# Optimization experiments

Measured on AMD Instinct MI355X. Metric: run time of the kernel, lower is better.

Reference implementation:

```python
import jax, jax.numpy as jnp
import numpy as np

N_SPANS = 2000
D_SPAN = 1220          # span representation dim (Test_Encoder docstring)
P = 65536              # number of (mention, antecedent) pairs
D_PHI = 60             # dist(20) + genre(20) + speaker(20)
IN_SIZE = 3 * D_SPAN + D_PHI  # 3720
HID = 150
BINS = np.array([1, 2, 3, 4, 5, 8, 16, 32, 64])


def setup_inputs() -> dict:
    key = jax.random.key(0)
    ks = jax.random.split(key, 16)
    inp = {
        "g_i": jax.random.normal(ks[0], (N_SPANS, D_SPAN), dtype=jnp.float32),
        "s_m": jax.random.normal(ks[1], (N_SPANS,), dtype=jnp.float32),
        "mention_ids": jax.random.randint(ks[2], (P,), 0, N_SPANS, dtype=jnp.int32),
        "antecedent_ids": jax.random.randint(ks[3], (P,), 0, N_SPANS, dtype=jnp.int32),
        "distances": jax.random.randint(ks[4], (P,), 1, 512, dtype=jnp.int32),
        "genres": jax.random.randint(ks[5], (P,), 0, 7, dtype=jnp.int32),
        "speakers": jax.random.randint(ks[6], (P,), 0, 3, dtype=jnp.int32),
        # embedding tables
        "dist_emb": jax.random.normal(ks[7], (len(BINS), 20), dtype=jnp.float32) * 0.1,
        "genre_emb": jax.random.normal(ks[8], (7, 20), dtype=jnp.float32) * 0.1,
        "speaker_emb": jax.random.normal(ks[9], (3, 20), dtype=jnp.float32) * 0.1,
        # FFNN params (fc1, fc2, fc3)
        "W1": jax.random.normal(ks[10], (IN_SIZE, HID), dtype=jnp.float32) / np.sqrt(IN_SIZE),
        "b1": jnp.zeros((HID,), dtype=jnp.float32),
        "W2": jax.random.normal(ks[11], (HID, HID), dtype=jnp.float32) / np.sqrt(HID),
        "b2": jnp.zeros((HID,), dtype=jnp.float32),
        "W3": jax.random.normal(ks[12], (HID, 1), dtype=jnp.float32) / np.sqrt(HID),
        "b3": jnp.zeros((1,), dtype=jnp.float32),
    }
    return inp


def _dist_to_bin(distances):
    # replicate Span_Distance_Embedding.dist_to_bin_id: bin id s.t. bins[id] <= d < bins[id+1],
    # last bin catches everything else (including d < 1, per the Python fallthrough).
    bins = jnp.asarray(BINS, dtype=jnp.int32)
    ids = jnp.searchsorted(bins, distances, side="right") - 1
    return jnp.clip(ids, 0, len(BINS) - 1)


def reference(g_i, s_m, mention_ids, antecedent_ids, distances, genres, speakers,
              dist_emb, genre_emb, speaker_emb, W1, b1, W2, b2, W3, b3):
    # phi_ij: concat of distance / genre / speaker embeddings   [P, 60]
    phi = jnp.concatenate(
        [dist_emb[_dist_to_bin(distances)], genre_emb[genres], speaker_emb[speakers]],
        axis=1)
    vec_i = g_i[mention_ids]        # [P, D]
    vec_j = g_i[antecedent_ids]     # [P, D]
    x = jnp.concatenate([vec_i, vec_j, vec_j * vec_j, phi], axis=1)  # [P, 3D+60]
    # FFNN (dropout inactive at eval)
    h = jax.nn.relu(x @ W1 + b1)
    h = jax.nn.relu(h @ W2 + b2)
    s_ij = (h @ W3 + b3)[:, 0]      # [P]
    coref_scores = s_m[mention_ids] + s_m[antecedent_ids] + s_ij
    return coref_scores
```

## Files before the change

### kernel.cpp

```cpp
#include <hip/hip_runtime.h>

typedef short bf16x8 __attribute__((ext_vector_type(8)));
typedef short bf16x4 __attribute__((ext_vector_type(4)));
typedef float f32x4  __attribute__((ext_vector_type(4)));

#define NSPAN 2000
#define DSPAN 1220
#define NPAIR 65536
#define HID   150
#define HP    160
#define TW    320
#define NKS   78
#define NKH   39
#define NMT   128
#define NNT   20
#define KC    6
#define NCMB  189

#define GA 1248
#define GB 390
#define GC 119
#define GD 13
#define GE 160

static __device__ __forceinline__ short f2bf(float x) {
  unsigned u = __builtin_bit_cast(unsigned, x);
  u = (u + 0x7FFFu + ((u >> 16) & 1u)) >> 16;
  return (short)u;
}

__global__ __launch_bounds__(256)
void prep_all(const float* __restrict__ g, const float* __restrict__ W1,
              const float* __restrict__ b1, const float* __restrict__ de,
              const float* __restrict__ ge, const float* __restrict__ se,
              const float* __restrict__ W2, short* __restrict__ A_fr,
              short* __restrict__ Wc_fr, float* __restrict__ combo,
              short* __restrict__ W2_fr, float* __restrict__ T) {
  int b = blockIdx.x;
  int t = threadIdx.x;
  if (b < GA) {
    int tid = b * 256 + t;
    int l  = tid & 63;
    int t2 = tid >> 6;
    int ks = t2 % NKH;
    int mt = t2 / NKH;
    int m  = mt * 16 + (l & 15);
    int k0 = ks * 32 + ((l >> 4) << 3);
    float x[8];
    if (m < NSPAN && k0 + 8 <= DSPAN) {
      float4 f0 = *(const float4*)&g[m * DSPAN + k0];
      float4 f1 = *(const float4*)&g[m * DSPAN + k0 + 4];
      x[0]=f0.x; x[1]=f0.y; x[2]=f0.z; x[3]=f0.w;
      x[4]=f1.x; x[5]=f1.y; x[6]=f1.z; x[7]=f1.w;
    } else {
#pragma unroll
      for (int i = 0; i < 8; ++i) {
        int k = k0 + i;
        x[i] = (m < NSPAN && k < DSPAN) ? g[m * DSPAN + k] : 0.f;
      }
    }
    short v1[8], v2[8];
#pragma unroll
    for (int i = 0; i < 8; ++i) { v1[i] = f2bf(x[i]); v2[i] = f2bf(x[i] * x[i]); }
    size_t o1 = ((size_t)(mt * NKS + ks) * 64 + l) * 8;
    *(bf16x8*)(A_fr + o1) = *(const bf16x8*)v1;
    *(bf16x8*)(A_fr + o1 + (size_t)NKH * 512) = *(const bf16x8*)v2;
  } else if (b < GA + GB) {
    int tid = (b - GA) * 256 + t;
    int l  = tid & 63;
    int t2 = tid >> 6;
    int ks = t2 % NKS;
    int nt = t2 / NKS;
    int n  = nt * 16 + (l & 15);
    int k0 = ks * 32 + ((l >> 4) << 3);
    short v[8];
#pragma unroll
    for (int i = 0; i < 8; ++i) {
      int k = k0 + i;
      float x = 0.f;
      if (n < HID) {
        if (k < DSPAN)                     x = W1[k * HID + n];
      } else if (n >= HP && n < HP + HID) {
        int j = n - HP;
        if (k < DSPAN)                     x = W1[(DSPAN + k) * HID + j];
        else if (k >= 1248 && k < 2468)    x = W1[(1192 + k) * HID + j];
      }
      v[i] = f2bf(x);
    }
    *(bf16x8*)(Wc_fr + (size_t)tid * 8) = *(const bf16x8*)v;
  } else if (b < GA + GB + GC) {
    int idx = (b - GA - GB) * 256 + t;
    if (idx < NCMB * HP) {
      int c = idx / HP;
      int j = idx - c * HP;
      float v = 0.f;
      if (j < HID) {
        int si = c % 3;
        int t2 = c / 3;
        int gi = t2 % 7;
        int bi = t2 / 7;
        v = b1[j];
        const float* dp = de + bi * 20;
        const float* gp = ge + gi * 20;
        const float* sp = se + si * 20;
#pragma unroll
        for (int e = 0; e < 20; ++e) {
          v += dp[e] * W1[(3660 + e) * HID + j];
          v += gp[e] * W1[(3680 + e) * HID + j];
          v += sp[e] * W1[(3700 + e) * HID + j];
        }
      }
      combo[idx] = v;
    }
  } else if (b < GA + GB + GC + GD) {
    int tid = (b - GA - GB - GC) * 256 + t;
    if (tid < 3200) {
      int l  = tid & 63;
      int t2 = tid >> 6;
      int ks = t2 % 5;
      int jt = t2 / 5;
      int n  = jt * 16 + (l & 15);
      int k0 = ks * 32 + ((l >> 4) << 3);
      short v[8];
#pragma unroll
      for (int i = 0; i < 8; ++i) {
        int k = k0 + i;
        float x = (k < HID && n < HID) ? W2[k * HID + n] : 0.f;
        v[i] = f2bf(x);
      }
      *(bf16x8*)(W2_fr + (size_t)tid * 8) = *(const bf16x8*)v;
    }
  } else {
    int idx = (b - GA - GB - GC - GD) * 256 + t;
    f32x4 z = {0.f, 0.f, 0.f, 0.f};
    if (idx < NSPAN * TW / 4) ((f32x4*)T)[idx] = z;
  }
}

__global__ __launch_bounds__(256)
void span_gemm(const short* __restrict__ A_fr, const short* __restrict__ Wc_fr,
               float* __restrict__ T) {
  int t = threadIdx.x, w = t >> 6, l = t & 63;
  int mt  = blockIdx.y * 4 + w;
  int ntb = blockIdx.x * 4;
  int ksb = blockIdx.z * 13;
  const short* pa = A_fr + ((size_t)(mt * NKS + ksb) * 64 + l) * 8;
  const short* pb = Wc_fr + ((size_t)(ntb * NKS + ksb) * 64 + l) * 8;
  f32x4 a0 = {0.f, 0.f, 0.f, 0.f}, a1 = a0, a2 = a0, a3 = a0;
#pragma unroll
  for (int ks = 0; ks < 13; ++ks) {
    bf16x8 a  = *(const bf16x8*)pa;
    bf16x8 b0 = *(const bf16x8*)pb;
    bf16x8 b1 = *(const bf16x8*)(pb + (size_t)NKS * 512);
    bf16x8 b2 = *(const bf16x8*)(pb + (size_t)2 * NKS * 512);
    bf16x8 b3 = *(const bf16x8*)(pb + (size_t)3 * NKS * 512);
    a0 = __builtin_amdgcn_mfma_f32_16x16x32_bf16(a, b0, a0, 0, 0, 0);
    a1 = __builtin_amdgcn_mfma_f32_16x16x32_bf16(a, b1, a1, 0, 0, 0);
    a2 = __builtin_amdgcn_mfma_f32_16x16x32_bf16(a, b2, a2, 0, 0, 0);
    a3 = __builtin_amdgcn_mfma_f32_16x16x32_bf16(a, b3, a3, 0, 0, 0);
    pa += 512; pb += 512;
  }
  int col = l & 15, row4 = (l >> 4) << 2;
  f32x4 acc[4] = {a0, a1, a2, a3};
#pragma unroll
  for (int r = 0; r < 4; ++r) {
    int m = mt * 16 + row4 + r;
    if (m < NSPAN) {
#pragma unroll
      for (int j = 0; j < 4; ++j)
        atomicAdd(&T[m * TW + (ntb + j) * 16 + col], acc[j][r]);
    }
  }
}

__global__ __launch_bounds__(256)
void pair_kernel(const float* __restrict__ T, const float* __restrict__ combo,
                 const short* __restrict__ W2_fr,
                 const float* __restrict__ b2, const float* __restrict__ W3,
                 const float* __restrict__ b3, const float* __restrict__ s_m,
                 const int* __restrict__ m_ids, const int* __restrict__ a_ids,
                 const int* __restrict__ dist, const int* __restrict__ genre,
                 const int* __restrict__ spk, float* __restrict__ out) {
  __shared__ float w3s[HP], b2s[HP], sm2[64];

  int t = threadIdx.x, w = t >> 6, l = t & 63;
  int base = blockIdx.x * 64;

  if (t < 64) {
    int p = base + t;
    sm2[t] = s_m[m_ids[p]] + s_m[a_ids[p]];
  }
  if (t < HP) {
    w3s[t] = (t < HID) ? W3[t] : 0.f;
    b2s[t] = (t < HID) ? b2[t] : 0.f;
  }
  float b3v = b3[0];
  __syncthreads();

  int pr = l & 15;
  int q  = l >> 4;
  int p  = base + w * 16 + pr;
  int m = m_ids[p], a = a_ids[p];
  int d = dist[p];
  int bb = (d >= 2) + (d >= 3) + (d >= 4) + (d >= 5) + (d >= 8) +
           (d >= 16) + (d >= 32) + (d >= 64);
  int co = ((bb * 7 + genre[p]) * 3 + spk[p]) * HP;

  const float* pA = T + m * TW + q * 8;
  const float* pB = T + a * TW + HP + q * 8;
  const float* pC = combo + co + q * 8;

  bf16x8 af[5];
#pragma unroll
  for (int ks = 0; ks < 5; ++ks) {
    float4 va0 = *(const float4*)(pA + ks * 32);
    float4 va1 = *(const float4*)(pA + ks * 32 + 4);
    float4 vb0 = *(const float4*)(pB + ks * 32);
    float4 vb1 = *(const float4*)(pB + ks * 32 + 4);
    float4 vc0 = *(const float4*)(pC + ks * 32);
    float4 vc1 = *(const float4*)(pC + ks * 32 + 4);
    short v[8];
    v[0] = f2bf(fmaxf(va0.x + vb0.x + vc0.x, 0.f));
    v[1] = f2bf(fmaxf(va0.y + vb0.y + vc0.y, 0.f));
    v[2] = f2bf(fmaxf(va0.z + vb0.z + vc0.z, 0.f));
    v[3] = f2bf(fmaxf(va0.w + vb0.w + vc0.w, 0.f));
    v[4] = f2bf(fmaxf(va1.x + vb1.x + vc1.x, 0.f));
    v[5] = f2bf(fmaxf(va1.y + vb1.y + vc1.y, 0.f));
    v[6] = f2bf(fmaxf(va1.z + vb1.z + vc1.z, 0.f));
    v[7] = f2bf(fmaxf(va1.w + vb1.w + vc1.w, 0.f));
    af[ks] = *(const bf16x8*)v;
  }

  f32x4 acc[10];
#pragma unroll
  for (int jt = 0; jt < 10; ++jt) acc[jt] = {0.f, 0.f, 0.f, 0.f};

  const short* pw = W2_fr + l * 8;
#pragma unroll
  for (int jt = 0; jt < 10; ++jt) {
#pragma unroll
    for (int ks = 0; ks < 5; ++ks) {
      bf16x8 bfr = *(const bf16x8*)(pw + (size_t)(jt * 5 + ks) * 512);
      acc[jt] = __builtin_amdgcn_mfma_f32_16x16x32_bf16(af[ks], bfr, acc[jt], 0, 0, 0);
    }
  }

  float part[4] = {0.f, 0.f, 0.f, 0.f};
  int cl = l & 15;
#pragma unroll
  for (int jt = 0; jt < 10; ++jt) {
    int n = jt * 16 + cl;
    float w3v = w3s[n], b2v = b2s[n];
#pragma unroll
    for (int r = 0; r < 4; ++r) part[r] += fmaxf(acc[jt][r] + b2v, 0.f) * w3v;
  }
#pragma unroll
  for (int off = 8; off >= 1; off >>= 1) {
#pragma unroll
    for (int r = 0; r < 4; ++r) part[r] += __shfl_xor(part[r], off, 64);
  }
  if (cl == 0) {
    int rowb = q << 2;
#pragma unroll
    for (int r = 0; r < 4; ++r) {
      int pl = w * 16 + rowb + r;
      out[base + pl] = sm2[pl] + part[r] + b3v;
    }
  }
}

extern "C" void kernel_launch(void* const* d_in, const int* in_sizes, int n_in,
                              void* d_out, int out_size, void* d_ws, size_t ws_size,
                              hipStream_t stream) {
  const float* g     = (const float*)d_in[0];
  const float* s_m   = (const float*)d_in[1];
  const int*   m_ids = (const int*)d_in[2];
  const int*   a_ids = (const int*)d_in[3];
  const int*   dist  = (const int*)d_in[4];
  const int*   genre = (const int*)d_in[5];
  const int*   spk   = (const int*)d_in[6];
  const float* de    = (const float*)d_in[7];
  const float* ge    = (const float*)d_in[8];
  const float* se    = (const float*)d_in[9];
  const float* W1    = (const float*)d_in[10];
  const float* b1    = (const float*)d_in[11];
  const float* W2    = (const float*)d_in[12];
  const float* b2    = (const float*)d_in[13];
  const float* W3    = (const float*)d_in[14];
  const float* b3    = (const float*)d_in[15];
  float* out = (float*)d_out;

  float* T     = (float*)d_ws;
  float* combo = T + NSPAN * TW;
  short* A_fr  = (short*)(combo + NCMB * HP);
  short* Wc_fr = A_fr + (size_t)NMT * NKS * 512;
  short* W2_fr = Wc_fr + (size_t)NNT * NKS * 512;

  prep_all<<<GA + GB + GC + GD + GE, 256, 0, stream>>>(
      g, W1, b1, de, ge, se, W2, A_fr, Wc_fr, combo, W2_fr, T);
  span_gemm<<<dim3(5, 32, KC), 256, 0, stream>>>(A_fr, Wc_fr, T);
  pair_kernel<<<NPAIR / 64, 256, 0, stream>>>(T, combo, W2_fr, b2, W3, b3, s_m,
                                              m_ids, a_ids, dist, genre, spk, out);
}
```

Measured before the change: 137.0 us.

## Store span projections and combo table in bf16 and deepen split-K

```diff
diff --git a/kernel.cpp b/kernel.cpp
--- a/kernel.cpp
+++ b/kernel.cpp
@@ -14,7 +14,7 @@
 #define NKH   39
 #define NMT   128
 #define NNT   20
-#define KC    6
+#define KC    13
 #define NCMB  189
 
 #define GA 1248
@@ -28,13 +28,17 @@
   u = (u + 0x7FFFu + ((u >> 16) & 1u)) >> 16;
   return (short)u;
 }
+static __device__ __forceinline__ float bf2f(short s) {
+  unsigned u = ((unsigned)(unsigned short)s) << 16;
+  return __builtin_bit_cast(float, u);
+}
 
 __global__ __launch_bounds__(256)
 void prep_all(const float* __restrict__ g, const float* __restrict__ W1,
               const float* __restrict__ b1, const float* __restrict__ de,
               const float* __restrict__ ge, const float* __restrict__ se,
               const float* __restrict__ W2, short* __restrict__ A_fr,
-              short* __restrict__ Wc_fr, float* __restrict__ combo,
+              short* __restrict__ Wc_fr, short* __restrict__ combo,
               short* __restrict__ W2_fr, float* __restrict__ T) {
   int b = blockIdx.x;
   int t = threadIdx.x;
@@ -110,7 +114,7 @@
           v += sp[e] * W1[(3700 + e) * HID + j];
         }
       }
-      combo[idx] = v;
+      combo[idx] = f2bf(v);
     }
   } else if (b < GA + GB + GC + GD) {
     int tid = (b - GA - GB - GC) * 256 + t;
@@ -143,12 +147,12 @@
   int t = threadIdx.x, w = t >> 6, l = t & 63;
   int mt  = blockIdx.y * 4 + w;
   int ntb = blockIdx.x * 4;
-  int ksb = blockIdx.z * 13;
+  int ksb = blockIdx.z * 6;
   const short* pa = A_fr + ((size_t)(mt * NKS + ksb) * 64 + l) * 8;
   const short* pb = Wc_fr + ((size_t)(ntb * NKS + ksb) * 64 + l) * 8;
   f32x4 a0 = {0.f, 0.f, 0.f, 0.f}, a1 = a0, a2 = a0, a3 = a0;
 #pragma unroll
-  for (int ks = 0; ks < 13; ++ks) {
+  for (int ks = 0; ks < 6; ++ks) {
     bf16x8 a  = *(const bf16x8*)pa;
     bf16x8 b0 = *(const bf16x8*)pb;
     bf16x8 b1 = *(const bf16x8*)(pb + (size_t)NKS * 512);
@@ -174,7 +178,16 @@
 }
 
 __global__ __launch_bounds__(256)
-void pair_kernel(const float* __restrict__ T, const float* __restrict__ combo,
+void convert_T(const float* __restrict__ Tf, short* __restrict__ Tb) {
+  int i = (blockIdx.x * 256 + threadIdx.x) * 4;
+  float4 v = *(const float4*)(Tf + i);
+  bf16x4 r;
+  r[0] = f2bf(v.x); r[1] = f2bf(v.y); r[2] = f2bf(v.z); r[3] = f2bf(v.w);
+  *(bf16x4*)(Tb + i) = r;
+}
+
+__global__ __launch_bounds__(256)
+void pair_kernel(const short* __restrict__ Tb, const short* __restrict__ combo,
                  const short* __restrict__ W2_fr,
                  const float* __restrict__ b2, const float* __restrict__ W3,
                  const float* __restrict__ b3, const float* __restrict__ s_m,
@@ -206,28 +219,20 @@
            (d >= 16) + (d >= 32) + (d >= 64);
   int co = ((bb * 7 + genre[p]) * 3 + spk[p]) * HP;
 
-  const float* pA = T + m * TW + q * 8;
-  const float* pB = T + a * TW + HP + q * 8;
-  const float* pC = combo + co + q * 8;
+  const short* pA = Tb + m * TW + q * 8;
+  const short* pB = Tb + a * TW + HP + q * 8;
+  const short* pC = combo + co + q * 8;
 
   bf16x8 af[5];
 #pragma unroll
   for (int ks = 0; ks < 5; ++ks) {
-    float4 va0 = *(const float4*)(pA + ks * 32);
-    float4 va1 = *(const float4*)(pA + ks * 32 + 4);
-    float4 vb0 = *(const float4*)(pB + ks * 32);
-    float4 vb1 = *(const float4*)(pB + ks * 32 + 4);
-    float4 vc0 = *(const float4*)(pC + ks * 32);
-    float4 vc1 = *(const float4*)(pC + ks * 32 + 4);
+    bf16x8 va = *(const bf16x8*)(pA + ks * 32);
+    bf16x8 vb = *(const bf16x8*)(pB + ks * 32);
+    bf16x8 vc = *(const bf16x8*)(pC + ks * 32);
     short v[8];
-    v[0] = f2bf(fmaxf(va0.x + vb0.x + vc0.x, 0.f));
-    v[1] = f2bf(fmaxf(va0.y + vb0.y + vc0.y, 0.f));
-    v[2] = f2bf(fmaxf(va0.z + vb0.z + vc0.z, 0.f));
-    v[3] = f2bf(fmaxf(va0.w + vb0.w + vc0.w, 0.f));
-    v[4] = f2bf(fmaxf(va1.x + vb1.x + vc1.x, 0.f));
-    v[5] = f2bf(fmaxf(va1.y + vb1.y + vc1.y, 0.f));
-    v[6] = f2bf(fmaxf(va1.z + vb1.z + vc1.z, 0.f));
-    v[7] = f2bf(fmaxf(va1.w + vb1.w + vc1.w, 0.f));
+#pragma unroll
+    for (int i = 0; i < 8; ++i)
+      v[i] = f2bf(fmaxf(bf2f(va[i]) + bf2f(vb[i]) + bf2f(vc[i]), 0.f));
     af[ks] = *(const bf16x8*)v;
   }
 
@@ -290,15 +295,17 @@
   const float* b3    = (const float*)d_in[15];
   float* out = (float*)d_out;
 
-  float* T     = (float*)d_ws;
-  float* combo = T + NSPAN * TW;
-  short* A_fr  = (short*)(combo + NCMB * HP);
+  float* Tf    = (float*)d_ws;
+  short* Tb    = (short*)(Tf + NSPAN * TW);
+  short* combo = Tb + NSPAN * TW;
+  short* A_fr  = combo + NCMB * HP;
   short* Wc_fr = A_fr + (size_t)NMT * NKS * 512;
   short* W2_fr = Wc_fr + (size_t)NNT * NKS * 512;
 
   prep_all<<<GA + GB + GC + GD + GE, 256, 0, stream>>>(
-      g, W1, b1, de, ge, se, W2, A_fr, Wc_fr, combo, W2_fr, T);
-  span_gemm<<<dim3(5, 32, KC), 256, 0, stream>>>(A_fr, Wc_fr, T);
-  pair_kernel<<<NPAIR / 64, 256, 0, stream>>>(T, combo, W2_fr, b2, W3, b3, s_m,
+      g, W1, b1, de, ge, se, W2, A_fr, Wc_fr, combo, W2_fr, Tf);
+  span_gemm<<<dim3(5, 32, KC), 256, 0, stream>>>(A_fr, Wc_fr, Tf);
+  convert_T<<<625, 256, 0, stream>>>(Tf, Tb);
+  pair_kernel<<<NPAIR / 64, 256, 0, stream>>>(Tb, combo, W2_fr, b2, W3, b3, s_m,
                                               m_ids, a_ids, dist, genre, spk, out);
 }
```

After: 142.7 us. 4.1% more time.
